# Kernel optimization log

Measured on AMD Instinct MI355X. Metric: run time of the kernel, lower is better.

The kernel has to match this reference:

```python
import jax, jax.numpy as jnp
import numpy as np

ALPHA = 0.3


def _maxsim_scores(q, d):
    # q: [B, N, D], d: [C, S, D] -> scores [B, C]
    # MaxSim: per (query b, doc c), sum over query tokens of max over doc tokens.
    sim = jnp.einsum('bnd,csd->bcns', q, d)  # [B, C, N, S]
    return sim.max(axis=3).sum(axis=2)       # [B, C]


def setup_inputs() -> dict:
    key = jax.random.key(0)
    k1, k2, k3, k4 = jax.random.split(key, 4)
    B, N, S, D = 64, 32, 1024, 128
    return {
        'query_embeddings': jax.random.normal(k1, (B, N, D), dtype=jnp.float32),
        'doc_embeddings': jax.random.normal(k2, (B, S, D), dtype=jnp.float32),
        'teacher_query_outputs': jax.random.normal(k3, (B, N, D), dtype=jnp.float32),
        'teacher_doc_outputs': jax.random.normal(k4, (B, S, D), dtype=jnp.float32),
    }


def reference(query_embeddings, doc_embeddings, teacher_query_outputs, teacher_doc_outputs):
    scores = _maxsim_scores(query_embeddings, doc_embeddings)  # [B, B]
    B = scores.shape[0]
    pos_scores = jnp.diag(scores)                               # [B]
    eye = jnp.eye(B, dtype=bool)
    s_masked = jnp.where(eye, -jnp.inf, scores)
    neg_scores = s_masked.max(axis=1)                           # hardest negative per query
    contrastive_loss = jax.nn.softplus(neg_scores - pos_scores).mean()

    teacher_scores = _maxsim_scores(teacher_query_outputs, teacher_doc_outputs)
    # Torch MSELoss on fp16-cast inputs: compute in fp16, then promote.
    diff16 = scores.astype(jnp.float16) - teacher_scores.astype(jnp.float16)
    mse_loss = jnp.mean(diff16 * diff16).astype(jnp.float32)

    return contrastive_loss + ALPHA * mse_loss
```

## Files before the change

kernel.cpp:

```cpp
#include <hip/hip_runtime.h>
#include <hip/hip_bf16.h>

typedef __attribute__((ext_vector_type(8))) short short8;
typedef __attribute__((ext_vector_type(4))) float floatx4;

#define B_SZ   64
#define N_TOK  32
#define S_TOK  1024
#define D_DIM  128
#define ALPHA  0.3f

#define STRIP_S     32
#define STRIP_EL    (STRIP_S * D_DIM)
#define STRIP_BYTES (STRIP_EL * 2)
#define NSTRIP      (S_TOK / STRIP_S)
#define C_EL        (S_TOK * D_DIM)

#define DBLK (B_SZ * S_TOK * D_DIM / 8 / 256)
#define QBLK (B_SZ * N_TOK * D_DIM / 8 / 256)

__device__ __forceinline__ short f2bf(float f) {
    __hip_bfloat16 h = __float2bfloat16(f);
    return __builtin_bit_cast(short, h);
}

__device__ __forceinline__ short8 cvt8(const float* __restrict__ p) {
    floatx4 f0 = *reinterpret_cast<const floatx4*>(p);
    floatx4 f1 = *reinterpret_cast<const floatx4*>(p + 4);
    short8 r;
    r[0] = f2bf(f0[0]); r[1] = f2bf(f0[1]); r[2] = f2bf(f0[2]); r[3] = f2bf(f0[3]);
    r[4] = f2bf(f1[0]); r[5] = f2bf(f1[1]); r[6] = f2bf(f1[2]); r[7] = f2bf(f1[3]);
    return r;
}

__global__ __launch_bounds__(256) void cvt_all_kernel(
    const float* __restrict__ q,  const float* __restrict__ d,
    const float* __restrict__ tq, const float* __restrict__ td,
    __hip_bfloat16* __restrict__ qb,  __hip_bfloat16* __restrict__ db,
    __hip_bfloat16* __restrict__ tqb, __hip_bfloat16* __restrict__ tdb) {
    const int which = blockIdx.y;
    if (blockIdx.x >= DBLK) {
        const float* src = which ? tq : q;
        __hip_bfloat16* dst = which ? tqb : qb;
        int idx = (blockIdx.x - DBLK) * 256 + threadIdx.x;
        *reinterpret_cast<short8*>(dst + (size_t)idx * 8) = cvt8(src + (size_t)idx * 8);
    } else {
        const float* src = which ? td : d;
        __hip_bfloat16* dst = which ? tdb : db;
        int idx = blockIdx.x * 256 + threadIdx.x;
        int kc = idx & 15;
        int s  = (idx >> 4) & (S_TOK - 1);
        int c  = idx >> 14;
        int st = s >> 5, nt = (s >> 4) & 1, lr = s & 15;
        int ks = kc >> 2, lg = kc & 3;
        size_t dpos = (size_t)c * C_EL + (size_t)st * STRIP_EL
                    + (size_t)(ks * 2 + nt) * 512 + (size_t)(lg * 16 + lr) * 8;
        *reinterpret_cast<short8*>(dst + dpos) = cvt8(src + (size_t)idx * 8);
    }
}

__device__ __forceinline__ void gload_lds16(const void* g, void* l) {
    __builtin_amdgcn_global_load_lds(
        (const __attribute__((address_space(1))) unsigned int*)g,
        (__attribute__((address_space(3))) unsigned int*)l, 16, 0, 0);
}

__global__ __launch_bounds__(256, 2) void maxsim_scores_kernel(
    const __hip_bfloat16* __restrict__ qb,  const __hip_bfloat16* __restrict__ db,
    const __hip_bfloat16* __restrict__ tqb, const __hip_bfloat16* __restrict__ tdb,
    float* __restrict__ scores_ws ) {

    const int c     = blockIdx.x;
    const int bg    = blockIdx.y;
    const int which = blockIdx.z;
    const __hip_bfloat16* Q = which ? tqb : qb;
    const __hip_bfloat16* D = which ? tdb : db;
    float* out = scores_ws + which * (B_SZ * B_SZ);

    const int tid = threadIdx.x;
    const int w   = tid >> 6;
    const int l   = tid & 63;
    const int lg  = l >> 4;
    const int lr  = l & 15;

    const int b0 = bg * 16 + w * 4;

    __shared__ __align__(16) char smem[2 * STRIP_BYTES];

    short8 afrag[8][4];
#pragma unroll
    for (int mt = 0; mt < 8; ++mt)
#pragma unroll
        for (int ks = 0; ks < 4; ++ks)
            afrag[mt][ks] = *reinterpret_cast<const short8*>(
                Q + ((size_t)(b0 + (mt >> 1)) * N_TOK + (mt & 1) * 16 + lr) * D_DIM
                  + ks * 32 + lg * 8);

    float runmax[8][4];
#pragma unroll
    for (int mt = 0; mt < 8; ++mt)
#pragma unroll
        for (int j = 0; j < 4; ++j) runmax[mt][j] = -INFINITY;

    const char* gstrip = (const char*)(D + (size_t)c * C_EL);
    const unsigned y0 = tid * 16;
    const unsigned y1 = 4096 + tid * 16;

    gload_lds16(gstrip + y0, smem + y0);
    gload_lds16(gstrip + y1, smem + y1);
    __syncthreads();

    for (int st = 0; st < NSTRIP; ++st) {
        const char* bufc = smem + (size_t)(st & 1) * STRIP_BYTES;

        if (st + 1 < NSTRIP) {
            const char* gs = gstrip + (size_t)(st + 1) * STRIP_BYTES;
            char* bufn = smem + (size_t)((st + 1) & 1) * STRIP_BYTES;
            gload_lds16(gs + y0, bufn + y0);
            gload_lds16(gs + y1, bufn + y1);
        }

#pragma unroll
        for (int nt = 0; nt < 2; ++nt) {
            short8 bf[4];
#pragma unroll
            for (int ks = 0; ks < 4; ++ks)
                bf[ks] = *reinterpret_cast<const short8*>(
                    bufc + (ks * 2 + nt) * 1024 + l * 16);

            floatx4 acc[8];
#pragma unroll
            for (int mt = 0; mt < 8; ++mt) acc[mt] = floatx4{0.f, 0.f, 0.f, 0.f};

#pragma unroll
            for (int ks = 0; ks < 4; ++ks)
#pragma unroll
                for (int mt = 0; mt < 8; ++mt)
                    acc[mt] = __builtin_amdgcn_mfma_f32_16x16x32_bf16(
                        afrag[mt][ks], bf[ks], acc[mt], 0, 0, 0);

#pragma unroll
            for (int mt = 0; mt < 8; ++mt)
#pragma unroll
                for (int j = 0; j < 4; ++j)
                    runmax[mt][j] = fmaxf(runmax[mt][j], acc[mt][j]);
        }

        __syncthreads();
    }

#pragma unroll
    for (int mt = 0; mt < 8; ++mt)
#pragma unroll
        for (int j = 0; j < 4; ++j) {
            float v = runmax[mt][j];
            v = fmaxf(v, __shfl_xor(v, 1));
            v = fmaxf(v, __shfl_xor(v, 2));
            v = fmaxf(v, __shfl_xor(v, 4));
            v = fmaxf(v, __shfl_xor(v, 8));
            runmax[mt][j] = v;
        }

#pragma unroll
    for (int p = 0; p < 4; ++p) {
        float s = 0.f;
#pragma unroll
        for (int j = 0; j < 4; ++j) s += runmax[2 * p][j] + runmax[2 * p + 1][j];
        s += __shfl_xor(s, 16);
        s += __shfl_xor(s, 32);
        if (l == 0) out[(b0 + p) * B_SZ + c] = s;
    }
}

__global__ void loss_kernel(const float* __restrict__ scores_ws, float* __restrict__ out) {
    const float* sc = scores_ws;
    const float* tc = scores_ws + B_SZ * B_SZ;
    const int b = threadIdx.x;

    float pos = sc[b * B_SZ + b];
    float neg = -INFINITY;
    float msesum = 0.f;
#pragma unroll 8
    for (int cc = 0; cc < B_SZ; ++cc) {
        float s = sc[b * B_SZ + cc];
        float t = tc[b * B_SZ + cc];
        if (cc != b) neg = fmaxf(neg, s);
        _Float16 d16 = (_Float16)s - (_Float16)t;
        _Float16 sq  = d16 * d16;
        msesum += (float)sq;
    }
    float x = neg - pos;
    float sp = (x > 0.f) ? (x + log1pf(expf(-x))) : log1pf(expf(x));

#pragma unroll
    for (int m = 1; m < 64; m <<= 1) {
        sp     += __shfl_xor(sp, m);
        msesum += __shfl_xor(msesum, m);
    }
    if (b == 0) {
        float mse = msesum / 4096.f;
        mse = (float)(_Float16)mse;
        out[0] = sp / 64.f + ALPHA * mse;
    }
}

extern "C" void kernel_launch(void* const* d_in, const int* in_sizes, int n_in,
                              void* d_out, int out_size, void* d_ws, size_t ws_size,
                              hipStream_t stream) {
    const float* q  = (const float*)d_in[0];
    const float* d  = (const float*)d_in[1];
    const float* tq = (const float*)d_in[2];
    const float* td = (const float*)d_in[3];
    float* out = (float*)d_out;

    const size_t QN = (size_t)B_SZ * N_TOK * D_DIM;
    const size_t DN = (size_t)B_SZ * S_TOK * D_DIM;

    float* scores_ws = (float*)d_ws;
    __hip_bfloat16* qb  = (__hip_bfloat16*)((char*)d_ws + 32768);
    __hip_bfloat16* tqb = qb + QN;
    __hip_bfloat16* db  = tqb + QN;
    __hip_bfloat16* tdb = db + DN;

    cvt_all_kernel<<<dim3(DBLK + QBLK, 2), 256, 0, stream>>>(
        q, d, tq, td, qb, db, tqb, tdb);

    dim3 grid(B_SZ, B_SZ / 16, 2);
    maxsim_scores_kernel<<<grid, 256, 0, stream>>>(qb, db, tqb, tdb, scores_ws);
    loss_kernel<<<1, 64, 0, stream>>>(scores_ws, out);
}
```

Before: 73.98 us.

## Deepen LDS prefetch pipeline to six buffers with vmcnt-based waits

Replaces the double-buffered strip loop with a six-buffer ring that prefetches three strips ahead, using explicit s_waitcnt vmcnt counts and a bare s_barrier per strip instead of __syncthreads. The goal is to hide more global-to-LDS latency and to avoid draining all outstanding loads at every barrier. The six-buffer ring means a buffer is not overwritten until three iterations after it was read, so the trailing barrier can be dropped. An empty asm pins the query fragments in registers. LDS use grows from 16KB to 48KB per block, which may limit occupancy at two blocks per CU.

```diff
diff --git a/kernel.cpp b/kernel.cpp
--- a/kernel.cpp
+++ b/kernel.cpp
@@ -14,10 +14,14 @@
 #define STRIP_EL    (STRIP_S * D_DIM)
 #define STRIP_BYTES (STRIP_EL * 2)
 #define NSTRIP      (S_TOK / STRIP_S)
+#define NBUF        6
 #define C_EL        (S_TOK * D_DIM)
 
 #define DBLK (B_SZ * S_TOK * D_DIM / 8 / 256)
 #define QBLK (B_SZ * N_TOK * D_DIM / 8 / 256)
+
+#define WAITV_(N) asm volatile("s_waitcnt vmcnt(" #N ")" ::: "memory")
+#define WAITV(N)  WAITV_(N)
 
 __device__ __forceinline__ short f2bf(float f) {
     __hip_bfloat16 h = __float2bfloat16(f);
@@ -85,7 +89,7 @@
 
     const int b0 = bg * 16 + w * 4;
 
-    __shared__ __align__(16) char smem[2 * STRIP_BYTES];
+    __shared__ __align__(16) char smem[NBUF * STRIP_BYTES];
 
     short8 afrag[8][4];
 #pragma unroll
@@ -95,6 +99,11 @@
             afrag[mt][ks] = *reinterpret_cast<const short8*>(
                 Q + ((size_t)(b0 + (mt >> 1)) * N_TOK + (mt & 1) * 16 + lr) * D_DIM
                   + ks * 32 + lg * 8);
+#pragma unroll
+    for (int mt = 0; mt < 8; ++mt)
+#pragma unroll
+        for (int ks = 0; ks < 4; ++ks)
+            asm volatile("" : "+v"(afrag[mt][ks]));
 
     float runmax[8][4];
 #pragma unroll
@@ -106,20 +115,13 @@
     const unsigned y0 = tid * 16;
     const unsigned y1 = 4096 + tid * 16;
 
-    gload_lds16(gstrip + y0, smem + y0);
-    gload_lds16(gstrip + y1, smem + y1);
-    __syncthreads();
-
-    for (int st = 0; st < NSTRIP; ++st) {
-        const char* bufc = smem + (size_t)(st & 1) * STRIP_BYTES;
-
-        if (st + 1 < NSTRIP) {
-            const char* gs = gstrip + (size_t)(st + 1) * STRIP_BYTES;
-            char* bufn = smem + (size_t)((st + 1) & 1) * STRIP_BYTES;
-            gload_lds16(gs + y0, bufn + y0);
-            gload_lds16(gs + y1, bufn + y1);
-        }
-
+#pragma unroll
+    for (int p = 0; p < 3; ++p) {
+        gload_lds16(gstrip + p * STRIP_BYTES + y0, smem + p * STRIP_BYTES + y0);
+        gload_lds16(gstrip + p * STRIP_BYTES + y1, smem + p * STRIP_BYTES + y1);
+    }
+
+    auto compute = [&](const char* bufc) {
 #pragma unroll
         for (int nt = 0; nt < 2; ++nt) {
             short8 bf[4];
@@ -145,9 +147,26 @@
                 for (int j = 0; j < 4; ++j)
                     runmax[mt][j] = fmaxf(runmax[mt][j], acc[mt][j]);
         }
-
-        __syncthreads();
-    }
+    };
+
+    for (int st = 0; st < NSTRIP - 3; ++st) {
+        const int tb = (st + 3) % NBUF;
+        const char* gs = gstrip + (size_t)(st + 3) * STRIP_BYTES;
+        gload_lds16(gs + y0, smem + tb * STRIP_BYTES + y0);
+        gload_lds16(gs + y1, smem + tb * STRIP_BYTES + y1);
+        WAITV(6);
+        __builtin_amdgcn_s_barrier();
+        compute(smem + (st % NBUF) * STRIP_BYTES);
+    }
+    WAITV(4);
+    __builtin_amdgcn_s_barrier();
+    compute(smem + ((NSTRIP - 3) % NBUF) * STRIP_BYTES);
+    WAITV(2);
+    __builtin_amdgcn_s_barrier();
+    compute(smem + ((NSTRIP - 2) % NBUF) * STRIP_BYTES);
+    WAITV(0);
+    __builtin_amdgcn_s_barrier();
+    compute(smem + ((NSTRIP - 1) % NBUF) * STRIP_BYTES);
 
 #pragma unroll
     for (int mt = 0; mt < 8; ++mt)
```

After: 74.45 us. No clear change (+0.6%).

## Load doc B-fragments directly from global into registers, drop LDS staging

Applied to the files above, without the earlier changes.

Replaces the double-buffered LDS strip pipeline (global_load_lds plus __syncthreads) with per-wave direct global loads of pre-swizzled B fragments into registers, software-pipelined with two register buffers. This removes the LDS round trip and the block-wide barriers. The cost is that each of the 4 waves now fetches the same doc strip separately from global/L2, which multiplies cache traffic. An empty asm pins the A fragments in registers.

```diff
diff --git a/kernel.cpp b/kernel.cpp
--- a/kernel.cpp
+++ b/kernel.cpp
@@ -59,12 +59,6 @@
     }
 }
 
-__device__ __forceinline__ void gload_lds16(const void* g, void* l) {
-    __builtin_amdgcn_global_load_lds(
-        (const __attribute__((address_space(1))) unsigned int*)g,
-        (__attribute__((address_space(3))) unsigned int*)l, 16, 0, 0);
-}
-
 __global__ __launch_bounds__(256, 2) void maxsim_scores_kernel(
     const __hip_bfloat16* __restrict__ qb,  const __hip_bfloat16* __restrict__ db,
     const __hip_bfloat16* __restrict__ tqb, const __hip_bfloat16* __restrict__ tdb,
@@ -85,8 +79,6 @@
 
     const int b0 = bg * 16 + w * 4;
 
-    __shared__ __align__(16) char smem[2 * STRIP_BYTES];
-
     short8 afrag[8][4];
 #pragma unroll
     for (int mt = 0; mt < 8; ++mt)
@@ -95,6 +87,11 @@
             afrag[mt][ks] = *reinterpret_cast<const short8*>(
                 Q + ((size_t)(b0 + (mt >> 1)) * N_TOK + (mt & 1) * 16 + lr) * D_DIM
                   + ks * 32 + lg * 8);
+#pragma unroll
+    for (int mt = 0; mt < 8; ++mt)
+#pragma unroll
+        for (int ks = 0; ks < 4; ++ks)
+            asm volatile("" : "+v"(afrag[mt][ks]));
 
     float runmax[8][4];
 #pragma unroll
@@ -102,52 +99,44 @@
 #pragma unroll
         for (int j = 0; j < 4; ++j) runmax[mt][j] = -INFINITY;
 
-    const char* gstrip = (const char*)(D + (size_t)c * C_EL);
-    const unsigned y0 = tid * 16;
-    const unsigned y1 = 4096 + tid * 16;
-
-    gload_lds16(gstrip + y0, smem + y0);
-    gload_lds16(gstrip + y1, smem + y1);
-    __syncthreads();
-
-    for (int st = 0; st < NSTRIP; ++st) {
-        const char* bufc = smem + (size_t)(st & 1) * STRIP_BYTES;
-
-        if (st + 1 < NSTRIP) {
-            const char* gs = gstrip + (size_t)(st + 1) * STRIP_BYTES;
-            char* bufn = smem + (size_t)((st + 1) & 1) * STRIP_BYTES;
-            gload_lds16(gs + y0, bufn + y0);
-            gload_lds16(gs + y1, bufn + y1);
-        }
-
-#pragma unroll
-        for (int nt = 0; nt < 2; ++nt) {
-            short8 bf[4];
-#pragma unroll
-            for (int ks = 0; ks < 4; ++ks)
-                bf[ks] = *reinterpret_cast<const short8*>(
-                    bufc + (ks * 2 + nt) * 1024 + l * 16);
-
-            floatx4 acc[8];
-#pragma unroll
-            for (int mt = 0; mt < 8; ++mt) acc[mt] = floatx4{0.f, 0.f, 0.f, 0.f};
-
-#pragma unroll
-            for (int ks = 0; ks < 4; ++ks)
-#pragma unroll
-                for (int mt = 0; mt < 8; ++mt)
-                    acc[mt] = __builtin_amdgcn_mfma_f32_16x16x32_bf16(
-                        afrag[mt][ks], bf[ks], acc[mt], 0, 0, 0);
-
+    const char* gbase = (const char*)(D + (size_t)c * C_EL) + l * 16;
+
+    auto load_phase = [&](short8 bb[4], int st, int nt) {
+        const char* p = gbase + (size_t)st * STRIP_BYTES + nt * 1024;
+#pragma unroll
+        for (int ks = 0; ks < 4; ++ks)
+            bb[ks] = *reinterpret_cast<const short8*>(p + ks * 2048);
+    };
+
+    auto compute = [&](const short8 bb[4]) {
+        floatx4 acc[8];
+#pragma unroll
+        for (int mt = 0; mt < 8; ++mt) acc[mt] = floatx4{0.f, 0.f, 0.f, 0.f};
+#pragma unroll
+        for (int ks = 0; ks < 4; ++ks)
 #pragma unroll
             for (int mt = 0; mt < 8; ++mt)
-#pragma unroll
-                for (int j = 0; j < 4; ++j)
-                    runmax[mt][j] = fmaxf(runmax[mt][j], acc[mt][j]);
-        }
-
-        __syncthreads();
-    }
+                acc[mt] = __builtin_amdgcn_mfma_f32_16x16x32_bf16(
+                    afrag[mt][ks], bb[ks], acc[mt], 0, 0, 0);
+#pragma unroll
+        for (int mt = 0; mt < 8; ++mt)
+#pragma unroll
+            for (int j = 0; j < 4; ++j)
+                runmax[mt][j] = fmaxf(runmax[mt][j], acc[mt][j]);
+    };
+
+    short8 bb0[4], bb1[4];
+    load_phase(bb0, 0, 0);
+
+    for (int st = 0; st < NSTRIP - 1; ++st) {
+        load_phase(bb1, st, 1);
+        compute(bb0);
+        load_phase(bb0, st + 1, 0);
+        compute(bb1);
+    }
+    load_phase(bb1, NSTRIP - 1, 1);
+    compute(bb0);
+    compute(bb1);
 
 #pragma unroll
     for (int mt = 0; mt < 8; ++mt)
```

After: 77.59 us. 4.9% more time.
